# Optimization experiments

Hardware: AMD Instinct MI355X
Metric: run time of the kernel (lower is better)

Reference implementation:

```python
import jax, jax.numpy as jnp
import numpy as np

H = 4                      # attention heads
L_NAMES = ['self', 'cross'] * 3
K_LIST = [None, None, 128, 128, 64, 64]  # top-k per layer (None = full attention)
BN_EPS = 1e-5


def conv1d(x, W, b):
    # 1x1 Conv1d: x [B, Ci, N], W [Co, Ci], b [Co]
    return jnp.einsum('oi,bin->bon', W, x) + b[:, None]


def bn_eval(x, g, b):
    # BatchNorm1d in eval mode with running mean 0 / var 1
    inv = 1.0 / np.sqrt(1.0 + BN_EPS)
    return (g * inv)[:, None] * x + b[:, None]


def mha(x, src, Wq, bq, Wk, bk, Wv, bv, Wm, bm, k):
    B, D, N = x.shape
    dh = D // H
    q = conv1d(x, Wq, bq).reshape(B, dh, H, N)
    kk = conv1d(src, Wk, bk).reshape(B, dh, H, -1)
    v = conv1d(src, Wv, bv).reshape(B, dh, H, -1)
    scores = jnp.einsum('bdhn,bdhm->bhnm', q, kk) / np.sqrt(dh)  # [B,H,N,M]
    if k is None:
        p = jax.nn.softmax(scores, axis=-1)
        out = jnp.einsum('bhnm,bdhm->bdhn', p, v)
    else:
        vals, idx = jax.lax.top_k(scores, k)          # [B,H,N,k]
        S = jax.nn.softmax(vals, axis=-1)
        # gather value vectors at the top-k key indices: [B,dh,H,N,k]
        vg = jnp.take_along_axis(v[:, :, :, None, :], idx[:, None, :, :, :], axis=4)
        out = jnp.einsum('bhnk,bdhnk->bdhn', S, vg)
    return conv1d(out.reshape(B, D, N), Wm, bm)


def log_ot(scores, alpha, iters):
    b, m, n = scores.shape
    bins0 = jnp.broadcast_to(alpha, (b, m, 1))
    bins1 = jnp.broadcast_to(alpha, (b, 1, n))
    a = jnp.broadcast_to(alpha, (b, 1, 1))
    Z0 = jnp.concatenate([jnp.concatenate([scores, bins0], -1),
                          jnp.concatenate([bins1, a], -1)], 1)  # [b,m+1,n+1]
    norm = -np.log(float(m + n))
    log_mu = jnp.concatenate([jnp.full((m,), norm, scores.dtype),
                              jnp.array([np.log(float(n)) + norm], scores.dtype)])
    log_nu = jnp.concatenate([jnp.full((n,), norm, scores.dtype),
                              jnp.array([np.log(float(m)) + norm], scores.dtype)])
    log_mu = jnp.broadcast_to(log_mu, (b, m + 1))
    log_nu = jnp.broadcast_to(log_nu, (b, n + 1))

    def step(carry, _):
        u, v = carry
        u = log_mu - jax.nn.logsumexp(Z0 + v[:, None, :], axis=2)
        v = log_nu - jax.nn.logsumexp(Z0 + u[:, :, None], axis=1)
        return (u, v), None

    (u, v), _ = jax.lax.scan(step, (jnp.zeros_like(log_mu), jnp.zeros_like(log_nu)),
                             None, length=iters)
    return Z0 + u[:, :, None] + v[:, None, :] - norm


def _forward(desc0, desc1, Wq, bq, Wk, bk, Wv, bv, Wm, bm,
             W1, b1, g1, be1, W2, b2, Wf, bf, alpha, iters):
    d0, d1 = desc0, desc1
    for i, (name, k) in enumerate(zip(L_NAMES, K_LIST)):
        s0, s1 = (d1, d0) if name == 'cross' else (d0, d1)

        def prop(x, src):
            msg = mha(x, src, Wq[i], bq[i], Wk[i], bk[i], Wv[i], bv[i], Wm[i], bm[i], k)
            h = jnp.concatenate([x, msg], axis=1)           # [B, 2D, N]
            h = jax.nn.relu(bn_eval(conv1d(h, W1[i], b1[i]), g1[i], be1[i]))
            return conv1d(h, W2[i], b2[i])

        dlt0, dlt1 = prop(d0, s0), prop(d1, s1)
        d0, d1 = d0 + dlt0, d1 + dlt1
    m0 = conv1d(d0, Wf, bf)
    m1 = conv1d(d1, Wf, bf)
    scores = jnp.einsum('bdn,bdm->bnm', m0, m1) / np.sqrt(m0.shape[1])
    return log_ot(scores, alpha, iters)


def setup_inputs() -> dict:
    B, D, N, L = 4, 128, 1024, 6
    key = jax.random.key(0)
    ks = jax.random.split(key, 20)

    def nrm(k, shape, s):
        return jax.random.normal(k, shape, jnp.float32) * s

    sw = 1.0 / np.sqrt(D)
    return {
        'desc0': nrm(ks[0], (B, D, N), 1.0),
        'desc1': nrm(ks[1], (B, D, N), 1.0),
        'Wq': nrm(ks[2], (L, D, D), sw), 'bq': jnp.zeros((L, D), jnp.float32),
        'Wk': nrm(ks[3], (L, D, D), sw), 'bk': jnp.zeros((L, D), jnp.float32),
        'Wv': nrm(ks[4], (L, D, D), sw), 'bv': jnp.zeros((L, D), jnp.float32),
        'Wm': nrm(ks[5], (L, D, D), sw), 'bm': jnp.zeros((L, D), jnp.float32),
        'W1': nrm(ks[6], (L, 2 * D, 2 * D), 1.0 / np.sqrt(2 * D)),
        'b1': jnp.zeros((L, 2 * D), jnp.float32),
        'g1': jnp.ones((L, 2 * D), jnp.float32),
        'be1': jnp.zeros((L, 2 * D), jnp.float32),
        'W2': nrm(ks[7], (L, D, 2 * D), 1.0 / np.sqrt(2 * D)),
        'b2': jnp.zeros((L, D), jnp.float32),
        'Wf': nrm(ks[8], (D, D), sw), 'bf': jnp.zeros((D,), jnp.float32),
        'alpha': jnp.asarray(1.0, jnp.float32),
        'iters': 20,
    }


def reference(desc0, desc1, Wq, bq, Wk, bk, Wv, bv, Wm, bm,
              W1, b1, g1, be1, W2, b2, Wf, bf, alpha, iters):
    return _forward(desc0, desc1, Wq, bq, Wk, bk, Wv, bv, Wm, bm,
                    W1, b1, g1, be1, W2, b2, Wf, bf, alpha, iters)
```

## Files before the change

### kernel.cpp

```cpp
#include <hip/hip_runtime.h>
#include <stdint.h>

#define NPOS   1024
#define DMODEL 128
#define NP1    1025
#define PLP    1053700
#define PSTR   1028
#define NORMF  (-7.624618986159398f)
#define LOGN   (6.931471805599453f)

typedef __attribute__((ext_vector_type(8))) short s8v;
typedef __attribute__((ext_vector_type(4))) float f4v;
typedef unsigned short ushort_t;

#define MFMA(a, b, c) __builtin_amdgcn_mfma_f32_16x16x32_bf16((a), (b), (c), 0, 0, 0)

static __device__ __forceinline__ ushort_t f2bf(float f) {
    union { float f; uint32_t u; } c; c.f = f;
    uint32_t u = c.u;
    return (ushort_t)((u + 0x7fffu + ((u >> 16) & 1u)) >> 16);
}
static __device__ __forceinline__ uint32_t cvtpk(float lo, float hi) {
    uint32_t r;
    asm("v_cvt_pk_bf16_f32 %0, %1, %2" : "=v"(r) : "v"(lo), "v"(hi));
    return r;
}

#define NW0 294912
#define NW1 98304
#define NW2 393216
#define NW3 196608
#define NW4 16384
#define NB5 2304
__global__ __launch_bounds__(256) void prep_weights(
    const float* __restrict__ Wq, const float* __restrict__ Wk, const float* __restrict__ Wv,
    const float* __restrict__ bq, const float* __restrict__ bk, const float* __restrict__ bv,
    const float* __restrict__ Wm, const float* __restrict__ W1, const float* __restrict__ W2,
    const float* __restrict__ Wf,
    ushort_t* __restrict__ wqkv, ushort_t* __restrict__ wm, ushort_t* __restrict__ w1,
    ushort_t* __restrict__ w2, ushort_t* __restrict__ wf, float* __restrict__ bqkv)
{
    int idx = blockIdx.x * 256 + threadIdx.x;
    if (idx < NW0) {
        int l = idx / 49152, r2 = idx % 49152;
        int r = r2 / 128, i = r2 % 128;
        int sel = r >> 7, rr = r & 127;
        int o = ((rr & 31) << 2) + (rr >> 5);
        const float* src = sel == 0 ? Wq : (sel == 1 ? Wk : Wv);
        wqkv[idx] = f2bf(src[((size_t)l * 128 + o) * 128 + i]);
        return;
    }
    idx -= NW0;
    if (idx < NW1) {
        int l = idx / 16384, o = (idx % 16384) / 128, ip = idx % 128;
        int i = ((ip & 31) << 2) + (ip >> 5);
        wm[idx] = f2bf(Wm[((size_t)l * 128 + o) * 128 + i]);
        return;
    }
    idx -= NW1;
    if (idx < NW2) { w1[idx] = f2bf(W1[idx]); return; }
    idx -= NW2;
    if (idx < NW3) { w2[idx] = f2bf(W2[idx]); return; }
    idx -= NW3;
    if (idx < NW4) { wf[idx] = f2bf(Wf[idx]); return; }
    idx -= NW4;
    if (idx < NB5) {
        int l = idx / 384, r = idx % 384;
        int sel = r >> 7, rr = r & 127;
        int o = ((rr & 31) << 2) + (rr >> 5);
        const float* src = sel == 0 ? bq : (sel == 1 ? bk : bv);
        bqkv[idx] = src[l * 128 + o];
    }
}

__global__ __launch_bounds__(256) void transpose_in(
    const float* __restrict__ desc0, const float* __restrict__ desc1,
    float* __restrict__ df, ushort_t* __restrict__ db)
{
    int g = blockIdx.z;
    int nb = blockIdx.x << 6, cb = blockIdx.y << 5;
    __shared__ float sm[32][65];
    const float* S = (g < 4 ? desc0 : desc1);
    int gl = g & 3;
    {
        int row = threadIdx.x >> 3, c8 = (threadIdx.x & 7) << 3;
        const float* p = S + ((size_t)gl * 128 + cb + row) * NPOS + nb + c8;
        float4 v0 = *(const float4*)p;
        float4 v1 = *(const float4*)(p + 4);
        sm[row][c8 + 0] = v0.x; sm[row][c8 + 1] = v0.y; sm[row][c8 + 2] = v0.z; sm[row][c8 + 3] = v0.w;
        sm[row][c8 + 4] = v1.x; sm[row][c8 + 5] = v1.y; sm[row][c8 + 6] = v1.z; sm[row][c8 + 7] = v1.w;
    }
    __syncthreads();
    int n = threadIdx.x >> 2, cc = (threadIdx.x & 3) << 3;
    float y[8];
    #pragma unroll
    for (int e = 0; e < 8; ++e) y[e] = sm[cc + e][n];
    size_t base = ((size_t)g * NPOS + nb + n) * DMODEL + cb + cc;
    *(float4*)(df + base) = make_float4(y[0], y[1], y[2], y[3]);
    *(float4*)(df + base + 4) = make_float4(y[4], y[5], y[6], y[7]);
    uint4 pk = make_uint4(cvtpk(y[0], y[1]), cvtpk(y[2], y[3]),
                          cvtpk(y[4], y[5]), cvtpk(y[6], y[7]));
    *(uint4*)(db + base) = pk;
}

__global__ __launch_bounds__(256) void conv_mfma(
    const ushort_t* __restrict__ X0, const ushort_t* __restrict__ X1, int c0, int Ci,
    const ushort_t* __restrict__ W, const float* __restrict__ bias,
    const float* __restrict__ bn_g, const float* __restrict__ bn_b,
    float* __restrict__ resid, ushort_t* __restrict__ outb, int Co, int mode)
{
    int g = blockIdx.z;
    int nb = blockIdx.x << 6;
    int obb = blockIdx.y << 6;
    int wave = threadIdx.x >> 6, lane = threadIdx.x & 63;
    int lrow = lane & 15, lk = (lane >> 4) << 3;
    int ob = obb + (wave << 4);
    f4v acc[4] = {};
    const ushort_t* wrow = W + (size_t)(ob + lrow) * Ci + lk;
    for (int k0 = 0; k0 < Ci; k0 += 32) {
        int k = k0 + lk;
        s8v b = *(const s8v*)(wrow + k0);
        #pragma unroll
        for (int t = 0; t < 4; ++t) {
            int n = nb + (t << 4) + lrow;
            const ushort_t* xp;
            if (k < c0) xp = X0 + ((size_t)g * NPOS + n) * c0 + k;
            else        xp = X1 + ((size_t)g * NPOS + n) * (Ci - c0) + (k - c0);
            s8v a = *(const s8v*)xp;
            acc[t] = MFMA(a, b, acc[t]);
        }
    }
    __shared__ float sm[64][68];
    #pragma unroll
    for (int t = 0; t < 4; ++t)
        #pragma unroll
        for (int r = 0; r < 4; ++r)
            sm[(t << 4) + ((lane >> 4) << 2) + r][(wave << 4) + lrow] = acc[t][r];
    __syncthreads();
    const float BN_INV = 0.9999950000374997f;
    int n = threadIdx.x >> 2, oc = (threadIdx.x & 3) << 4;
    int o0 = obb + oc;
    float y[16];
    #pragma unroll
    for (int e = 0; e < 16; ++e) y[e] = sm[n][oc + e] + bias[o0 + e];
    size_t base = ((size_t)g * NPOS + nb + n) * Co + o0;
    if (mode == 1) {
        #pragma unroll
        for (int e = 0; e < 16; ++e)
            y[e] = fmaxf(bn_g[o0 + e] * BN_INV * y[e] + bn_b[o0 + e], 0.f);
    } else if (mode == 2) {
        float* rp = resid + base;
        #pragma unroll
        for (int q = 0; q < 16; q += 4) {
            float4 r4 = *(const float4*)(rp + q);
            y[q] += r4.x; y[q + 1] += r4.y; y[q + 2] += r4.z; y[q + 3] += r4.w;
            *(float4*)(rp + q) = make_float4(y[q], y[q + 1], y[q + 2], y[q + 3]);
        }
    }
    uint4 p0 = make_uint4(cvtpk(y[0], y[1]), cvtpk(y[2], y[3]),
                          cvtpk(y[4], y[5]), cvtpk(y[6], y[7]));
    uint4 p1 = make_uint4(cvtpk(y[8], y[9]), cvtpk(y[10], y[11]),
                          cvtpk(y[12], y[13]), cvtpk(y[14], y[15]));
    *(uint4*)(outb + base) = p0;
    *(uint4*)(outb + base + 8) = p1;
}

__global__ __launch_bounds__(256) void qkv_mfma(
    const ushort_t* __restrict__ X, const ushort_t* __restrict__ W,
    const float* __restrict__ bias,
    ushort_t* __restrict__ Qb, ushort_t* __restrict__ Kb, ushort_t* __restrict__ Vb)
{
    int g = blockIdx.z;
    int nb = blockIdx.x << 6;
    int obb = blockIdx.y << 6;
    int wave = threadIdx.x >> 6, lane = threadIdx.x & 63;
    int lrow = lane & 15, lk = (lane >> 4) << 3;
    int ob = obb + (wave << 4);
    f4v acc[4] = {};
    const ushort_t* wrow = W + (size_t)(ob + lrow) * DMODEL + lk;
    for (int k0 = 0; k0 < DMODEL; k0 += 32) {
        s8v b = *(const s8v*)(wrow + k0);
        #pragma unroll
        for (int t = 0; t < 4; ++t) {
            int n = nb + (t << 4) + lrow;
            s8v a = *(const s8v*)(X + ((size_t)g * NPOS + n) * DMODEL + k0 + lk);
            acc[t] = MFMA(a, b, acc[t]);
        }
    }
    __shared__ float sm[64][68];
    #pragma unroll
    for (int t = 0; t < 4; ++t)
        #pragma unroll
        for (int r = 0; r < 4; ++r)
            sm[(t << 4) + ((lane >> 4) << 2) + r][(wave << 4) + lrow] = acc[t][r];
    __syncthreads();
    if (obb < 256) {
        int n = threadIdx.x >> 2, oc = (threadIdx.x & 3) << 4;
        int ov = obb + oc;
        ushort_t* dst = (ov < 128) ? Qb : Kb;
        int c = ov & 127;
        float y[16];
        #pragma unroll
        for (int e = 0; e < 16; ++e) y[e] = sm[n][oc + e] + bias[ov + e];
        size_t base = ((size_t)g * NPOS + nb + n) * DMODEL + c;
        uint4 p0 = make_uint4(cvtpk(y[0], y[1]), cvtpk(y[2], y[3]),
                              cvtpk(y[4], y[5]), cvtpk(y[6], y[7]));
        uint4 p1 = make_uint4(cvtpk(y[8], y[9]), cvtpk(y[10], y[11]),
                              cvtpk(y[12], y[13]), cvtpk(y[14], y[15]));
        *(uint4*)(dst + base) = p0;
        *(uint4*)(dst + base + 8) = p1;
    } else {
        int c = threadIdx.x >> 2, mc = (threadIdx.x & 3) << 4;
        float bc = bias[obb + c];
        float y[16];
        #pragma unroll
        for (int e = 0; e < 16; ++e) y[e] = sm[mc + e][c] + bc;
        size_t base = ((size_t)g * DMODEL + (obb - 256) + c) * NPOS + nb + mc;
        uint4 p0 = make_uint4(cvtpk(y[0], y[1]), cvtpk(y[2], y[3]),
                              cvtpk(y[4], y[5]), cvtpk(y[6], y[7]));
        uint4 p1 = make_uint4(cvtpk(y[8], y[9]), cvtpk(y[10], y[11]),
                              cvtpk(y[12], y[13]), cvtpk(y[14], y[15]));
        *(uint4*)(Vb + base) = p0;
        *(uint4*)(Vb + base + 8) = p1;
    }
}

__global__ __launch_bounds__(256) void attn_fused(
    const ushort_t* __restrict__ Qb, const ushort_t* __restrict__ Kb,
    const ushort_t* __restrict__ Vb, ushort_t* __restrict__ ao,
    int k, int cross)
{
    __shared__ ushort_t sc[16 * 1024];
    int gh = blockIdx.y;
    int g = gh >> 2, h = gh & 3;
    int g2 = cross ? (g ^ 4) : g;
    int n0 = blockIdx.x << 4;
    int wave = threadIdx.x >> 6, lane = threadIdx.x & 63;
    int lrow = lane & 15, lq = lane >> 4;

    {
        int kq = wave;
        s8v qa = *(const s8v*)(Qb + ((size_t)g * NPOS + n0 + lrow) * DMODEL
                               + (h << 5) + (lq << 3));
        const float scale = 0.17677669529663687f;
        int swz = (lrow & 7) << 4;
        for (int mt = 0; mt < 16; ++mt) {
            int m = (kq << 8) + (mt << 4);
            s8v kb = *(const s8v*)(Kb + ((size_t)g2 * NPOS + m + lrow) * DMODEL
                                   + (h << 5) + (lq << 3));
            f4v z = {};
            z = MFMA(kb, qa, z);
            uint32_t p0 = cvtpk(z[0] * scale, z[1] * scale);
            uint32_t p1 = cvtpk(z[2] * scale, z[3] * scale);
            int byte = ((lrow << 11) + ((m + (lq << 2)) << 1)) ^ swz;
            *(uint2*)((char*)sc + byte) = make_uint2(p0, p1);
        }
    }
    __syncthreads();

    {
        bool dosel = (k < NPOS);
        for (int rr = 0; rr < 4; ++rr) {
            int row = (wave << 2) + rr;
            int swz = (row & 7) << 4;
            int base = (row << 11) + (lane << 5);
            uint4 d0 = *(const uint4*)((const char*)sc + (base ^ swz));
            uint4 d1 = *(const uint4*)((const char*)sc + ((base + 16) ^ swz));
            uint32_t wd[8] = {d0.x, d0.y, d0.z, d0.w, d1.x, d1.y, d1.z, d1.w};
            float val[16];
            #pragma unroll
            for (int q = 0; q < 8; ++q) {
                union { unsigned ui; float f; } c0, c1;
                c0.ui = wd[q] << 16; c1.ui = wd[q] & 0xFFFF0000u;
                val[2 * q] = c0.f; val[2 * q + 1] = c1.f;
            }
            float mx = val[0];
            #pragma unroll
            for (int t = 1; t < 16; ++t) mx = fmaxf(mx, val[t]);
            #pragma unroll
            for (int o = 32; o; o >>= 1) mx = fmaxf(mx, __shfl_xor(mx, o));

            bool sel[16];
            if (dosel) {
                unsigned prefix = 0;
                bool exact = false;
                for (int bit = 15; bit >= 0 && !exact; --bit) {
                    unsigned cand = prefix | (1u << bit);
                    unsigned craw = (cand & 0x8000u) ? (cand ^ 0x8000u) : (cand ^ 0xFFFFu);
                    union { unsigned ui; float f; } cf; cf.ui = craw << 16;
                    float cf_f = cf.f;
                    int c = 0;
                    #pragma unroll
                    for (int t = 0; t < 16; ++t)
                        c += __popcll(__ballot(val[t] >= cf_f));
                    if (c >= k) { prefix = cand; exact = (c == k); }
                }
                unsigned praw = (prefix & 0x8000u) ? (prefix ^ 0x8000u) : (prefix ^ 0xFFFFu);
                union { unsigned ui; float f; } pf; pf.ui = praw << 16;
                float thr = pf.f;
                if (exact) {
                    #pragma unroll
                    for (int t = 0; t < 16; ++t) sel[t] = (val[t] >= thr);
                } else {
                    int cgt = 0;
                    #pragma unroll
                    for (int t = 0; t < 16; ++t)
                        cgt += __popcll(__ballot(val[t] > thr));
                    int need = k - cgt;
                    unsigned long long lmask = (1ull << lane) - 1ull;
                    int before = 0;
                    #pragma unroll
                    for (int t = 0; t < 16; ++t)
                        before += __popcll(__ballot(val[t] == thr) & lmask);
                    int loc = 0;
                    #pragma unroll
                    for (int t = 0; t < 16; ++t) {
                        bool tie = (val[t] == thr);
                        sel[t] = (val[t] > thr) || (tie && (before + loc < need));
                        loc += tie ? 1 : 0;
                    }
                }
            } else {
                #pragma unroll
                for (int t = 0; t < 16; ++t) sel[t] = true;
            }
            float w[16], sum = 0.f;
            #pragma unroll
            for (int t = 0; t < 16; ++t) {
                w[t] = sel[t] ? __expf(val[t] - mx) : 0.f;
                sum += w[t];
            }
            #pragma unroll
            for (int o = 32; o; o >>= 1) sum += __shfl_xor(sum, o);
            float inv = 1.f / sum;
            uint32_t ow[8];
            #pragma unroll
            for (int q = 0; q < 8; ++q)
                ow[q] = cvtpk(w[2 * q] * inv, w[2 * q + 1] * inv);
            *(uint4*)((char*)sc + (base ^ swz)) = make_uint4(ow[0], ow[1], ow[2], ow[3]);
            *(uint4*)((char*)sc + ((base + 16) ^ swz)) = make_uint4(ow[4], ow[5], ow[6], ow[7]);
        }
    }
    __syncthreads();

    {
        int khalf = wave >> 1, dimg = wave & 1;
        int db = dimg << 4;
        int pswz = (lrow & 7) << 4;
        int pbase = (lrow << 11) + (khalf << 10) + (lq << 4);
        const ushort_t* vbase = Vb + ((size_t)g2 * DMODEL + (h << 5) + db + lrow) * NPOS
                                + (khalf << 9) + (lq << 3);
        f4v acc = {};
        #pragma unroll
        for (int ks = 0; ks < 16; ++ks) {
            s8v pa = *(const s8v*)((const char*)sc + ((pbase + (ks << 6)) ^ pswz));
            s8v vv = *(const s8v*)(vbase + (ks << 5));
            acc = MFMA(pa, vv, acc);
        }
        __syncthreads();
        if (khalf == 1)
            *(f4v*)((char*)sc + (((dimg << 6) + lane) << 4)) = acc;
        __syncthreads();
        if (khalf == 0) {
            f4v other = *(const f4v*)((char*)sc + (((dimg << 6) + lane) << 4));
            acc = acc + other;
            #pragma unroll
            for (int r = 0; r < 4; ++r) {
                int n = n0 + (lq << 2) + r;
                ao[((size_t)g * NPOS + n) * DMODEL + (h << 5) + db + lrow] = f2bf(acc[r]);
            }
        }
    }
}

__global__ __launch_bounds__(256) void final_mfma(
    const ushort_t* __restrict__ md, float* __restrict__ Z0P, float* __restrict__ Z0T)
{
    int b = blockIdx.z;
    int wave = threadIdx.x >> 6, lane = threadIdx.x & 63;
    int wr = wave >> 1, wc = wave & 1;
    int n0 = (blockIdx.y << 7) + (wr << 6);
    int m0 = (blockIdx.x << 7) + (wc << 6);
    int lrow = lane & 15, lk = (lane >> 4) << 3;
    f4v acc[4][4] = {};
    for (int k0 = 0; k0 < DMODEL; k0 += 32) {
        s8v qa[4], kb[4];
        #pragma unroll
        for (int t = 0; t < 4; ++t) {
            qa[t] = *(const s8v*)(md + ((size_t)b * NPOS + n0 + (t << 4) + lrow) * DMODEL + k0 + lk);
            kb[t] = *(const s8v*)(md + ((size_t)(b + 4) * NPOS + m0 + (t << 4) + lrow) * DMODEL + k0 + lk);
        }
        #pragma unroll
        for (int tn = 0; tn < 4; ++tn)
            #pragma unroll
            for (int tm = 0; tm < 4; ++tm)
                acc[tn][tm] = MFMA(qa[tn], kb[tm], acc[tn][tm]);
    }
    const float scf = 0.08838834764831845f;
    int rbase = (lane >> 4) << 2;
    #pragma unroll
    for (int tn = 0; tn < 4; ++tn) {
        #pragma unroll
        for (int tm = 0; tm < 4; ++tm) {
            #pragma unroll
            for (int r = 0; r < 4; ++r) {
                int n = n0 + (tn << 4) + rbase + r;
                int m = m0 + (tm << 4) + lrow;
                float y = acc[tn][tm][r] * scf;
                Z0P[(size_t)b * PLP + (size_t)n * PSTR + m] = y;
                Z0T[(size_t)b * PLP + (size_t)m * PSTR + n] = y;
            }
        }
    }
}

__global__ __launch_bounds__(1024) void ot_init(
    float* __restrict__ Z0P, float* __restrict__ Z0T, float* __restrict__ v,
    const float* __restrict__ alpha)
{
    float a = *alpha;
    int b = blockIdx.x, t = threadIdx.x;
    Z0P[(size_t)b * PLP + (size_t)t * PSTR + 1024] = a;
    Z0P[(size_t)b * PLP + (size_t)1024 * PSTR + t] = a;
    Z0T[(size_t)b * PLP + (size_t)t * PSTR + 1024] = a;
    Z0T[(size_t)b * PLP + (size_t)1024 * PSTR + t] = a;
    v[b * NP1 + t] = 0.f;
    if (t == 0) {
        Z0P[(size_t)b * PLP + (size_t)1024 * PSTR + 1024] = a;
        Z0T[(size_t)b * PLP + (size_t)1024 * PSTR + 1024] = a;
        v[b * NP1 + 1024] = 0.f;
    }
}

__global__ __launch_bounds__(256) void lse_sweep(
    const float* __restrict__ Z, const float* __restrict__ vin,
    float* __restrict__ uout)
{
    int wv = threadIdx.x >> 6, lane = threadIdx.x & 63;
    int r = blockIdx.x * 4 + wv;
    int b = r / NP1, i = r - b * NP1;
    const float* z  = Z + (size_t)b * PLP + (size_t)i * PSTR;
    const float* vb = vin + b * NP1;
    float x[17];
    #pragma unroll
    for (int t = 0; t < 4; ++t) {
        int j = ((t << 6) + lane) << 2;
        float4 zz = *(const float4*)(z + j);
        float4 vv = *(const float4*)(vb + j);
        x[4 * t + 0] = zz.x + vv.x;
        x[4 * t + 1] = zz.y + vv.y;
        x[4 * t + 2] = zz.z + vv.z;
        x[4 * t + 3] = zz.w + vv.w;
    }
    x[16] = (lane == 0) ? (z[1024] + vb[1024]) : -1e30f;
    float m = x[0];
    #pragma unroll
    for (int t = 1; t < 17; ++t) m = fmaxf(m, x[t]);
    #pragma unroll
    for (int o = 32; o; o >>= 1) m = fmaxf(m, __shfl_xor(m, o));
    float sum = 0.f;
    #pragma unroll
    for (int t = 0; t < 17; ++t) sum += __expf(x[t] - m);
    #pragma unroll
    for (int o = 32; o; o >>= 1) sum += __shfl_xor(sum, o);
    if (lane == 0)
        uout[b * NP1 + i] = NORMF + ((i == 1024) ? LOGN : 0.f) - (m + __logf(sum));
}

__global__ __launch_bounds__(256) void ot_final(
    float* __restrict__ out, const float* __restrict__ Z0P,
    const float* __restrict__ u, const float* __restrict__ v)
{
    int r = blockIdx.x;
    int b = r / NP1, i = r - b * NP1;
    float ui = u[b * NP1 + i] - NORMF;
    const float* zp = Z0P + (size_t)b * PLP + (size_t)i * PSTR;
    float* zo = out + ((size_t)b * NP1 + i) * NP1;
    const float* vb = v + b * NP1;
    for (int j = threadIdx.x; j < NP1; j += 256) zo[j] = zp[j] + ui + vb[j];
}

extern "C" void kernel_launch(void* const* d_in, const int* in_sizes, int n_in,
                              void* d_out, int out_size, void* d_ws, size_t ws_size,
                              hipStream_t stream)
{
    (void)in_sizes; (void)n_in; (void)out_size; (void)ws_size;
    const float* desc0 = (const float*)d_in[0];
    const float* desc1 = (const float*)d_in[1];
    const float* Wq = (const float*)d_in[2];  const float* bq = (const float*)d_in[3];
    const float* Wk = (const float*)d_in[4];  const float* bk = (const float*)d_in[5];
    const float* Wv = (const float*)d_in[6];  const float* bv = (const float*)d_in[7];
    const float* Wm = (const float*)d_in[8];  const float* bm = (const float*)d_in[9];
    const float* W1 = (const float*)d_in[10]; const float* b1 = (const float*)d_in[11];
    const float* g1 = (const float*)d_in[12]; const float* be1 = (const float*)d_in[13];
    const float* W2 = (const float*)d_in[14]; const float* b2 = (const float*)d_in[15];
    const float* Wf = (const float*)d_in[16]; const float* bf = (const float*)d_in[17];
    const float* alpha = (const float*)d_in[18];

    float* Zout = (float*)d_out;
    float* ws = (float*)d_ws;
    size_t o = 0;
    float* d_f32      = ws;                          o += 1048576;
    ushort_t* d_bf    = (ushort_t*)(ws + o);         o += 524288;
    ushort_t* Qb      = (ushort_t*)(ws + o);         o += 524288;
    ushort_t* Kb      = (ushort_t*)(ws + o);         o += 524288;
    ushort_t* Vb      = (ushort_t*)(ws + o);         o += 524288;
    ushort_t* aob     = (ushort_t*)(ws + o);         o += 524288;
    ushort_t* msgb    = (ushort_t*)(ws + o);         o += 524288;
    ushort_t* hb      = (ushort_t*)(ws + o);         o += 1048576;
    ushort_t* mdesc   = (ushort_t*)(ws + o);         o += 524288;
    ushort_t* wqkv    = (ushort_t*)(ws + o);         o += 147456;
    ushort_t* wmw     = (ushort_t*)(ws + o);         o += 49152;
    ushort_t* w1w     = (ushort_t*)(ws + o);         o += 196608;
    ushort_t* w2w     = (ushort_t*)(ws + o);         o += 98304;
    ushort_t* wfw     = (ushort_t*)(ws + o);         o += 8192;
    float* bqkv       = ws + o;                      o += 2304;
    float* ub         = ws + o;                      o += 4352;
    float* vb         = ws + o;                      o += 4352;
    float* Z0P        = ws + o;                      o += 4214800;
    float* Z0T        = ws + o;                      o += 4214800;

    dim3 blk(256);
    prep_weights<<<dim3((NW0 + NW1 + NW2 + NW3 + NW4 + NB5 + 255) / 256), blk, 0, stream>>>(
        Wq, Wk, Wv, bq, bk, bv, Wm, W1, W2, Wf, wqkv, wmw, w1w, w2w, wfw, bqkv);
    transpose_in<<<dim3(16, 4, 8), blk, 0, stream>>>(desc0, desc1, d_f32, d_bf);

    static const int KLIST[6] = {1024, 1024, 128, 128, 64, 64};
    for (int l = 0; l < 6; ++l) {
        int cross = l & 1;
        int k = KLIST[l];
        qkv_mfma<<<dim3(16, 6, 8), blk, 0, stream>>>(
            d_bf, wqkv + (size_t)l * 49152, bqkv + l * 384, Qb, Kb, Vb);
        attn_fused<<<dim3(64, 32), blk, 0, stream>>>(Qb, Kb, Vb, aob, k, cross);
        conv_mfma<<<dim3(16, 2, 8), blk, 0, stream>>>(
            aob, (const ushort_t*)nullptr, 128, 128, wmw + (size_t)l * 16384,
            bm + l * 128, nullptr, nullptr, nullptr, msgb, 128, 0);
        conv_mfma<<<dim3(16, 4, 8), blk, 0, stream>>>(
            d_bf, msgb, 128, 256, w1w + (size_t)l * 65536,
            b1 + l * 256, g1 + l * 256, be1 + l * 256, nullptr, hb, 256, 1);
        conv_mfma<<<dim3(16, 2, 8), blk, 0, stream>>>(
            hb, (const ushort_t*)nullptr, 256, 256, w2w + (size_t)l * 32768,
            b2 + l * 128, nullptr, nullptr, d_f32, d_bf, 128, 2);
    }
    conv_mfma<<<dim3(16, 2, 8), blk, 0, stream>>>(
        d_bf, (const ushort_t*)nullptr, 128, 128, wfw, bf,
        nullptr, nullptr, nullptr, mdesc, 128, 0);
    final_mfma<<<dim3(8, 8, 4), blk, 0, stream>>>(mdesc, Z0P, Z0T);
    ot_init<<<dim3(4), dim3(1024), 0, stream>>>(Z0P, Z0T, vb, alpha);
    for (int it = 0; it < 20; ++it) {
        lse_sweep<<<dim3(1025), blk, 0, stream>>>(Z0P, vb, ub);
        lse_sweep<<<dim3(1025), blk, 0, stream>>>(Z0T, ub, vb);
    }
    ot_final<<<dim3(4100), blk, 0, stream>>>(Zout, Z0P, ub, vb);
}
```

Measured before the change: 791.4 us.

## Store Sinkhorn score matrices in fp16 and raise priority around attention MFMA loops

The score matrix and its transpose used by the 40 logsumexp sweeps are now stored in half precision, with padded strides, instead of fp32. This halves the bytes each sweep reads. The fp32 copy is kept only for the final output. The attention kernel also wraps its MFMA loops in s_setprio to favour matrix issue. The risk is fp16 rounding in the Sinkhorn inputs, which adds error to u and v.

New measurement: 785.2 us. Within noise of the previous version (-0.8%).

```diff
diff --git a/kernel.cpp b/kernel.cpp
--- a/kernel.cpp
+++ b/kernel.cpp
@@ -1,4 +1,5 @@
 #include <hip/hip_runtime.h>
+#include <hip/hip_fp16.h>
 #include <stdint.h>
 
 #define NPOS   1024
@@ -6,6 +7,8 @@
 #define NP1    1025
 #define PLP    1053700
 #define PSTR   1028
+#define PLPH   1057800
+#define PSTRH  1032
 #define NORMF  (-7.624618986159398f)
 #define LOGN   (6.931471805599453f)
 
@@ -244,6 +247,7 @@
                                + (h << 5) + (lq << 3));
         const float scale = 0.17677669529663687f;
         int swz = (lrow & 7) << 4;
+        __builtin_amdgcn_s_setprio(1);
         for (int mt = 0; mt < 16; ++mt) {
             int m = (kq << 8) + (mt << 4);
             s8v kb = *(const s8v*)(Kb + ((size_t)g2 * NPOS + m + lrow) * DMODEL
@@ -255,6 +259,7 @@
             int byte = ((lrow << 11) + ((m + (lq << 2)) << 1)) ^ swz;
             *(uint2*)((char*)sc + byte) = make_uint2(p0, p1);
         }
+        __builtin_amdgcn_s_setprio(0);
     }
     __syncthreads();
 
@@ -351,12 +356,14 @@
         const ushort_t* vbase = Vb + ((size_t)g2 * DMODEL + (h << 5) + db + lrow) * NPOS
                                 + (khalf << 9) + (lq << 3);
         f4v acc = {};
+        __builtin_amdgcn_s_setprio(1);
         #pragma unroll
         for (int ks = 0; ks < 16; ++ks) {
             s8v pa = *(const s8v*)((const char*)sc + ((pbase + (ks << 6)) ^ pswz));
             s8v vv = *(const s8v*)(vbase + (ks << 5));
             acc = MFMA(pa, vv, acc);
         }
+        __builtin_amdgcn_s_setprio(0);
         __syncthreads();
         if (khalf == 1)
             *(f4v*)((char*)sc + (((dimg << 6) + lane) << 4)) = acc;
@@ -374,7 +381,8 @@
 }
 
 __global__ __launch_bounds__(256) void final_mfma(
-    const ushort_t* __restrict__ md, float* __restrict__ Z0P, float* __restrict__ Z0T)
+    const ushort_t* __restrict__ md, float* __restrict__ Z0P,
+    __half* __restrict__ Z0H, __half* __restrict__ Z0TH)
 {
     int b = blockIdx.z;
     int wave = threadIdx.x >> 6, lane = threadIdx.x & 63;
@@ -408,51 +416,63 @@
                 int m = m0 + (tm << 4) + lrow;
                 float y = acc[tn][tm][r] * scf;
                 Z0P[(size_t)b * PLP + (size_t)n * PSTR + m] = y;
-                Z0T[(size_t)b * PLP + (size_t)m * PSTR + n] = y;
+                __half hy = __float2half(y);
+                Z0H [(size_t)b * PLPH + (size_t)n * PSTRH + m] = hy;
+                Z0TH[(size_t)b * PLPH + (size_t)m * PSTRH + n] = hy;
             }
         }
     }
 }
 
 __global__ __launch_bounds__(1024) void ot_init(
-    float* __restrict__ Z0P, float* __restrict__ Z0T, float* __restrict__ v,
-    const float* __restrict__ alpha)
+    float* __restrict__ Z0P, __half* __restrict__ Z0H, __half* __restrict__ Z0TH,
+    float* __restrict__ v, const float* __restrict__ alpha)
 {
     float a = *alpha;
+    __half ha = __float2half(a);
     int b = blockIdx.x, t = threadIdx.x;
-    Z0P[(size_t)b * PLP + (size_t)t * PSTR + 1024] = a;
-    Z0P[(size_t)b * PLP + (size_t)1024 * PSTR + t] = a;
-    Z0T[(size_t)b * PLP + (size_t)t * PSTR + 1024] = a;
-    Z0T[(size_t)b * PLP + (size_t)1024 * PSTR + t] = a;
+    Z0P [(size_t)b * PLP  + (size_t)t * PSTR  + 1024] = a;
+    Z0P [(size_t)b * PLP  + (size_t)1024 * PSTR + t] = a;
+    Z0H [(size_t)b * PLPH + (size_t)t * PSTRH + 1024] = ha;
+    Z0H [(size_t)b * PLPH + (size_t)1024 * PSTRH + t] = ha;
+    Z0TH[(size_t)b * PLPH + (size_t)t * PSTRH + 1024] = ha;
+    Z0TH[(size_t)b * PLPH + (size_t)1024 * PSTRH + t] = ha;
     v[b * NP1 + t] = 0.f;
     if (t == 0) {
-        Z0P[(size_t)b * PLP + (size_t)1024 * PSTR + 1024] = a;
-        Z0T[(size_t)b * PLP + (size_t)1024 * PSTR + 1024] = a;
+        Z0P [(size_t)b * PLP  + (size_t)1024 * PSTR  + 1024] = a;
+        Z0H [(size_t)b * PLPH + (size_t)1024 * PSTRH + 1024] = ha;
+        Z0TH[(size_t)b * PLPH + (size_t)1024 * PSTRH + 1024] = ha;
         v[b * NP1 + 1024] = 0.f;
     }
 }
 
-__global__ __launch_bounds__(256) void lse_sweep(
-    const float* __restrict__ Z, const float* __restrict__ vin,
+__global__ __launch_bounds__(256) void lse_sweep_h(
+    const __half* __restrict__ Z, const float* __restrict__ vin,
     float* __restrict__ uout)
 {
     int wv = threadIdx.x >> 6, lane = threadIdx.x & 63;
     int r = blockIdx.x * 4 + wv;
     int b = r / NP1, i = r - b * NP1;
-    const float* z  = Z + (size_t)b * PLP + (size_t)i * PSTR;
+    const __half* z  = Z + (size_t)b * PLPH + (size_t)i * PSTRH;
     const float* vb = vin + b * NP1;
     float x[17];
     #pragma unroll
-    for (int t = 0; t < 4; ++t) {
-        int j = ((t << 6) + lane) << 2;
-        float4 zz = *(const float4*)(z + j);
-        float4 vv = *(const float4*)(vb + j);
-        x[4 * t + 0] = zz.x + vv.x;
-        x[4 * t + 1] = zz.y + vv.y;
-        x[4 * t + 2] = zz.z + vv.z;
-        x[4 * t + 3] = zz.w + vv.w;
-    }
-    x[16] = (lane == 0) ? (z[1024] + vb[1024]) : -1e30f;
+    for (int t = 0; t < 2; ++t) {
+        int j = (t << 9) + (lane << 3);
+        union { uint4 u; __half h[8]; } U;
+        U.u = *(const uint4*)(z + j);
+        float4 v0 = *(const float4*)(vb + j);
+        float4 v1 = *(const float4*)(vb + j + 4);
+        x[t * 8 + 0] = __half2float(U.h[0]) + v0.x;
+        x[t * 8 + 1] = __half2float(U.h[1]) + v0.y;
+        x[t * 8 + 2] = __half2float(U.h[2]) + v0.z;
+        x[t * 8 + 3] = __half2float(U.h[3]) + v0.w;
+        x[t * 8 + 4] = __half2float(U.h[4]) + v1.x;
+        x[t * 8 + 5] = __half2float(U.h[5]) + v1.y;
+        x[t * 8 + 6] = __half2float(U.h[6]) + v1.z;
+        x[t * 8 + 7] = __half2float(U.h[7]) + v1.w;
+    }
+    x[16] = (lane == 0) ? (__half2float(z[1024]) + vb[1024]) : -1e30f;
     float m = x[0];
     #pragma unroll
     for (int t = 1; t < 17; ++t) m = fmaxf(m, x[t]);
@@ -518,7 +538,8 @@
     float* ub         = ws + o;                      o += 4352;
     float* vb         = ws + o;                      o += 4352;
     float* Z0P        = ws + o;                      o += 4214800;
-    float* Z0T        = ws + o;                      o += 4214800;
+    __half* Z0H       = (__half*)(ws + o);           o += 2115600;
+    __half* Z0TH      = (__half*)(ws + o);           o += 2115600;
 
     dim3 blk(256);
     prep_weights<<<dim3((NW0 + NW1 + NW2 + NW3 + NW4 + NB5 + 255) / 256), blk, 0, stream>>>(
@@ -545,11 +566,11 @@
     conv_mfma<<<dim3(16, 2, 8), blk, 0, stream>>>(
         d_bf, (const ushort_t*)nullptr, 128, 128, wfw, bf,
         nullptr, nullptr, nullptr, mdesc, 128, 0);
-    final_mfma<<<dim3(8, 8, 4), blk, 0, stream>>>(mdesc, Z0P, Z0T);
-    ot_init<<<dim3(4), dim3(1024), 0, stream>>>(Z0P, Z0T, vb, alpha);
+    final_mfma<<<dim3(8, 8, 4), blk, 0, stream>>>(mdesc, Z0P, Z0H, Z0TH);
+    ot_init<<<dim3(4), dim3(1024), 0, stream>>>(Z0P, Z0H, Z0TH, vb, alpha);
     for (int it = 0; it < 20; ++it) {
-        lse_sweep<<<dim3(1025), blk, 0, stream>>>(Z0P, vb, ub);
-        lse_sweep<<<dim3(1025), blk, 0, stream>>>(Z0T, ub, vb);
+        lse_sweep_h<<<dim3(1025), blk, 0, stream>>>(Z0H,  vb, ub);
+        lse_sweep_h<<<dim3(1025), blk, 0, stream>>>(Z0TH, ub, vb);
     }
     ot_final<<<dim3(4100), blk, 0, stream>>>(Zout, Z0P, ub, vb);
 }
```
